# Performance work log

Measured on AMD Instinct MI355X. Metric: run time of the kernel, lower is better.

Reference implementation:

```python
import jax, jax.numpy as jnp
import numpy as np

N = 20000   # nodes per type (lnc and dis)
E = 160000  # edges per meta-path graph and per pos/neg link graph
H = 8       # attention heads
D = 32      # out_size per head (H*D = 256 flattened)
HID = 256   # hidden_size from ResNet projection


def _bn(x, g, b, eps=1e-5):
    # training-mode BatchNorm1d (biased variance, like torch)
    m = x.mean(0)
    v = x.var(0)
    return g * (x - m) * jax.lax.rsqrt(v + eps) + b


def _leaky(x, slope):
    return jnp.where(x >= 0, x, slope * x)


def _gat(h_src, h_dst, src, dst, W, al, ar, n_dst):
    # DGL GATConv (bipartite, shared fc, no bias, eval mode)
    fs = (h_src @ W).reshape(-1, H, D)          # [Ns,H,D]
    fd = (h_dst @ W).reshape(-1, H, D)          # [Nd,H,D]
    el = (fs * al).sum(-1)                      # [Ns,H]
    er = (fd * ar).sum(-1)                      # [Nd,H]
    e = _leaky(el[src] + er[dst], 0.2)          # [E,H]
    emax = jax.ops.segment_max(e, dst, num_segments=n_dst)
    emax = jnp.where(jnp.isfinite(emax), emax, 0.0)   # zero in-degree safety
    ee = jnp.exp(e - emax[dst])
    den = jax.ops.segment_sum(ee, dst, num_segments=n_dst)
    a = ee / jnp.maximum(den[dst], 1e-9)        # edge softmax over incoming edges
    out = jax.ops.segment_sum(a[:, :, None] * fs[src], dst, num_segments=n_dst)
    return _leaky(out, 0.01).reshape(n_dst, H * D)  # activation=F.leaky_relu, flatten(1)


def _sem_attn(z, W1, b1, w2):
    # z: [N, 2, H*D]; SemanticAttention
    w = (jnp.tanh(z @ W1 + b1) @ w2).mean(0)    # [2]
    beta = jax.nn.softmax(w, axis=0)            # [2]
    return (beta[None, :, None] * z).sum(1)     # [N, H*D]


def setup_inputs() -> dict:
    key = jax.random.key(0)
    ks = jax.random.split(key, 32)
    s = 0.05
    inp = {
        "x_lnc": jax.random.normal(ks[0], (N, 256), jnp.float32),
        "x_dis": jax.random.normal(ks[1], (N, 256), jnp.float32),
        "proj_W": jax.random.normal(ks[2], (2, 256, HID), jnp.float32) * s,
        "proj_bn_g": jnp.ones((HID,), jnp.float32),
        "proj_bn_b": jnp.zeros((HID,), jnp.float32),
        "short_W": jax.random.normal(ks[3], (2, 256, HID), jnp.float32) * s,
        "short_b": jnp.zeros((2, HID), jnp.float32),
        "gat_W": jax.random.normal(ks[4], (4, HID, H * D), jnp.float32) * s,
        "gat_al": jax.random.normal(ks[5], (4, H, D), jnp.float32) * s,
        "gat_ar": jax.random.normal(ks[6], (4, H, D), jnp.float32) * s,
        "sem_W1": jax.random.normal(ks[7], (H * D, 128), jnp.float32) * s,
        "sem_b1": jnp.zeros((128,), jnp.float32),
        "sem_w2": jax.random.normal(ks[8], (128,), jnp.float32) * s,
    }
    names = ["ld_src", "ld_dst", "ll_src", "ll_dst", "dl_src", "dl_dst",
             "dd_src", "dd_dst", "pos_src", "pos_dst", "neg_src", "neg_dst"]
    for i, nm in enumerate(names):
        inp[nm] = jax.random.randint(ks[10 + i], (E,), 0, N, jnp.int32)
    return inp


def reference(x_lnc, x_dis, proj_W, proj_bn_g, proj_bn_b, short_W, short_b,
              gat_W, gat_al, gat_ar, sem_W1, sem_b1, sem_w2,
              ld_src, ld_dst, ll_src, ll_dst, dl_src, dl_dst,
              dd_src, dd_dst, pos_src, pos_dst, neg_src, neg_dst):
    # ResNet projection (shared BN applied per-branch, training-mode stats)
    l_x = _leaky(_bn(x_lnc @ proj_W[0], proj_bn_g, proj_bn_b), 0.01) + (x_lnc @ short_W[0] + short_b[0])
    d_x = _leaky(_bn(x_dis @ proj_W[1], proj_bn_g, proj_bn_b), 0.01) + (x_dis @ short_W[1] + short_b[1])
    # HANLayer: 4 meta-path GATs with pairings (l,d),(l,l),(d,l),(d,d)
    e0 = _gat(l_x, d_x, ld_src, ld_dst, gat_W[0], gat_al[0], gat_ar[0], N)  # dst dis
    e1 = _gat(l_x, l_x, ll_src, ll_dst, gat_W[1], gat_al[1], gat_ar[1], N)  # dst lnc
    e2 = _gat(d_x, l_x, dl_src, dl_dst, gat_W[2], gat_al[2], gat_ar[2], N)  # dst lnc
    e3 = _gat(d_x, d_x, dd_src, dd_dst, gat_W[3], gat_al[3], gat_ar[3], N)  # dst dis
    l_embs = _sem_attn(jnp.stack((e1, e2), axis=1), sem_W1, sem_b1, sem_w2)
    d_embs = _sem_attn(jnp.stack((e0, e3), axis=1), sem_W1, sem_b1, sem_w2)
    # Hadamard u_mul_v over 'lnc-dis' edges (pos graph and neg graph)
    pos_z = l_embs[pos_src] * d_embs[pos_dst]
    neg_z = l_embs[neg_src] * d_embs[neg_dst]
    return pos_z, neg_z, l_embs, d_embs
```

## Files before the change

### kernel.cpp

```cpp
#include <hip/hip_runtime.h>
#include <math.h>

#define NN 20000
#define NE 160000
#define SLOT 40

typedef _Float16 f16;
typedef __attribute__((ext_vector_type(8))) _Float16 f16x8;
typedef __attribute__((ext_vector_type(4))) float f32x4;

__device__ __forceinline__ float leakyf(float x, float s){ return x >= 0.f ? x : s*x; }
__device__ __forceinline__ ushort f2h(float x){ f16 h = (f16)x; ushort u; __builtin_memcpy(&u,&h,2); return u; }
__device__ __forceinline__ float h2f(ushort u){ f16 h; __builtin_memcpy(&h,&u,2); return (float)h; }

__device__ __forceinline__ void gload_lds16(const void* g, void* l){
  __builtin_amdgcn_global_load_lds((const __attribute__((address_space(1))) uint*)g,
                                   (__attribute__((address_space(3))) uint*)l, 16, 0, 0);
}

__global__ __launch_bounds__(256) void prep(const float* __restrict__ x_lnc,
    const float* __restrict__ x_dis, const float* __restrict__ proj_W,
    const float* __restrict__ short_W, const float* __restrict__ gat_W,
    const float* __restrict__ sem_W1,
    ushort* __restrict__ xhl, ushort* __restrict__ xhd,
    ushort* btpl, ushort* btpd, ushort* btgl, ushort* btgd, ushort* btsm,
    int* __restrict__ zbuf){
  int b = blockIdx.x;
  if (b < 10000){
    const float* in = (b >= 5000) ? x_dis : x_lnc;
    ushort* out = (b >= 5000) ? xhd : xhl;
    long idx = (long)(b % 5000)*256 + threadIdx.x;
    long r = idx>>6; int c4 = (int)(idx&63)<<2;
    float4 v = *(const float4*)(in + r*256 + c4);
    ushort4 o; o.x=f2h(v.x); o.y=f2h(v.y); o.z=f2h(v.z); o.w=f2h(v.w);
    *(ushort4*)(out + r*256 + c4) = o;
  } else if (b < 12688){
    int idx = (b-10000)*256 + threadIdx.x;
    float v; ushort* out; int n, k;
    if (idx < 131072){
      n = idx>>8; k = idx&255; out = btpl;
      v = (n<256)? proj_W[(size_t)k*256+n] : short_W[(size_t)k*256+(n-256)];
    } else if (idx < 262144){
      int l = idx-131072; n = l>>8; k = l&255; out = btpd;
      v = (n<256)? proj_W[65536+(size_t)k*256+n] : short_W[65536+(size_t)k*256+(n-256)];
    } else if (idx < 458752){
      int l = idx-262144; n = l>>8; k = l&255; out = btgl;
      int sl = n>>8; const float* bb = gat_W + (sl==0?0:(sl==1?65536:131072));
      v = bb[(size_t)k*256 + (n&255)];
    } else if (idx < 655360){
      int l = idx-458752; n = l>>8; k = l&255; out = btgd;
      int sl = n>>8; const float* bb = gat_W + (sl==0?0:(sl==1?131072:196608));
      v = bb[(size_t)k*256 + (n&255)];
    } else {
      int l = idx-655360; n = l>>8; k = l&255; out = btsm;
      v = sem_W1[(size_t)k*128 + n];
    }
    out[(size_t)n*256 + k] = f2h(v);
  } else {
    int idx = (b-12688)*256 + threadIdx.x;
    if (idx < 81028) zbuf[idx] = 0;
  }
}

__global__ void scatter_slots(const int* s0, const int* s1, const int* s2, const int* s3,
    const int* d0, const int* d1, const int* d2, const int* d3,
    int* __restrict__ cnt, int* __restrict__ slots){
  int g = blockIdx.y;
  const int* src = (g==0)?s0:(g==1)?s1:(g==2)?s2:s3;
  const int* dst = (g==0)?d0:(g==1)?d1:(g==2)?d2:d3;
  int i = blockIdx.x*256 + threadIdx.x;
  if (i<NE){
    int d = dst[i];
    int p = atomicAdd(&cnt[g*NN + d], 1);
    slots[(size_t)(g*NN + d)*SLOT + p] = src[i];
  }
}

template<int EPI>
__global__ __launch_bounds__(256) void gemm16(
    const ushort* __restrict__ A0, const ushort* __restrict__ A1,
    const ushort* __restrict__ B0, const ushort* __restrict__ B1,
    ushort* __restrict__ C0, ushort* __restrict__ C1, int ldc, int M,
    float* __restrict__ sbuf,
    const float* __restrict__ gat_al, const float* __restrict__ gat_ar,
    float* __restrict__ elbase, float* __restrict__ erbase,
    const float* __restrict__ b1v, const float* __restrict__ w2v){
  const int z = blockIdx.z;
  const ushort* A = z ? A1 : A0;
  const ushort* Bt = z ? B1 : B0;
  ushort* C = z ? C1 : C0;
  __shared__ ushort sm[16384];
  char* smc = (char*)sm;
  const int tid = threadIdx.x;
  const int lane = tid & 63, wid = tid >> 6;
  const int wr = wid >> 1, wc = wid & 1;
  const int fr = lane & 15, fq = lane >> 4;
  const int brow = blockIdx.y*128, bcol = blockIdx.x*128;
  f32x4 acc[4][4];
  #pragma unroll
  for (int i=0;i<4;i++)
    #pragma unroll
    for (int j=0;j<4;j++) acc[i][j] = (f32x4){0.f,0.f,0.f,0.f};

  for (int k0 = 0; k0 < 256; k0 += 64){
    __syncthreads();
    #pragma unroll
    for (int cc = 0; cc < 8; cc++){
      int c = wid*8 + cc;
      int ch = c & 15;
      int rel = ch*1024 + lane*16;
      int row = rel >> 7;
      int scb = (rel & 127) ^ ((row & 7) << 4);
      const char* src;
      if (c < 16){
        int gr = brow + row; gr = (gr < M) ? gr : (M-1);
        src = (const char*)A + (size_t)gr*512 + k0*2 + scb;
      } else {
        src = (const char*)Bt + (size_t)(bcol + row)*512 + k0*2 + scb;
      }
      gload_lds16(src, smc + ((c<16)?0:16384) + ch*1024);
    }
    __syncthreads();
    #pragma unroll
    for (int ks = 0; ks < 2; ks++){
      f16x8 af[4], bfr[4];
      #pragma unroll
      for (int i=0;i<4;i++){
        int r = wr*64 + i*16 + fr;
        int koff = ks*32 + fq*8;
        int aoff = ((r<<7) + koff*2) ^ ((r&7)<<4);
        af[i] = *(const f16x8*)(smc + aoff);
        int n = wc*64 + i*16 + fr;
        int boff = ((n<<7) + koff*2) ^ ((n&7)<<4);
        bfr[i] = *(const f16x8*)(smc + 16384 + boff);
      }
      #pragma unroll
      for (int i=0;i<4;i++)
        #pragma unroll
        for (int j=0;j<4;j++)
          acc[i][j] = __builtin_amdgcn_mfma_f32_16x16x32_f16(af[i], bfr[j], acc[i][j], 0,0,0);
    }
  }

  if (EPI==1 || EPI==2){
    #pragma unroll
    for (int i=0;i<4;i++){
      #pragma unroll
      for (int e=0;e<4;e++){
        int gr = brow + wr*64 + i*16 + fq*4 + e;
        if (gr < M){
          #pragma unroll
          for (int j=0;j<4;j++)
            C[(size_t)gr*ldc + bcol + wc*64 + j*16 + fr] = f2h(acc[i][j][e]);
        }
      }
    }
  }

  if (EPI==1 && bcol < 256){
    float* gsum = sbuf + z*512;
    float* gsq  = gsum + 256;
    #pragma unroll
    for (int j=0;j<4;j++){
      float s=0.f, q=0.f;
      #pragma unroll
      for (int i=0;i<4;i++)
        #pragma unroll
        for (int e=0;e<4;e++){
          int gr = brow + wr*64 + i*16 + fq*4 + e;
          if (gr < M){ float v = acc[i][j][e]; s += v; q += v*v; }
        }
      s += __shfl_xor(s,16); s += __shfl_xor(s,32);
      q += __shfl_xor(q,16); q += __shfl_xor(q,32);
      if (fq==0){
        int gc = bcol + wc*64 + j*16 + fr;
        atomicAdd(&gsum[gc], s);
        atomicAdd(&gsq[gc], q);
      }
    }
  }

  if (EPI==2){
    int slice = bcol >> 8;
    int hbase = (bcol & 255) >> 5;
    float *d1=nullptr, *d2=nullptr; const float *a1=nullptr, *a2=nullptr;
    if (z==0){
      if (slice==0){ d1=elbase; a1=gat_al; }
      else if (slice==1){ d1=elbase+160000; a1=gat_al+256; d2=erbase+160000; a2=gat_ar+256; }
      else { d1=erbase+320000; a1=gat_ar+512; }
    } else {
      if (slice==0){ d1=erbase; a1=gat_ar; }
      else if (slice==1){ d1=elbase+320000; a1=gat_al+512; }
      else { d1=elbase+480000; a1=gat_al+768; d2=erbase+480000; a2=gat_ar+768; }
    }
    int hA = hbase + wc*2, hB = hA+1;
    #pragma unroll
    for (int t=0;t<2;t++){
      const float* av = t ? a2 : a1;
      float* dst = t ? d2 : d1;
      if (t==1 && d2==nullptr) break;
      float avv[4];
      #pragma unroll
      for (int j=0;j<4;j++)
        avv[j] = av[(hbase + wc*2 + (j>>1))*32 + (j&1)*16 + fr];
      #pragma unroll
      for (int i=0;i<4;i++){
        #pragma unroll
        for (int e=0;e<4;e++){
          int gr = brow + wr*64 + i*16 + fq*4 + e;
          float pA = acc[i][0][e]*avv[0] + acc[i][1][e]*avv[1];
          float pB = acc[i][2][e]*avv[2] + acc[i][3][e]*avv[3];
          pA += __shfl_xor(pA,1); pA += __shfl_xor(pA,2);
          pA += __shfl_xor(pA,4); pA += __shfl_xor(pA,8);
          pB += __shfl_xor(pB,1); pB += __shfl_xor(pB,2);
          pB += __shfl_xor(pB,4); pB += __shfl_xor(pB,8);
          if (fr==0 && gr < M){
            dst[(size_t)gr*8 + hA] = pA;
            dst[(size_t)gr*8 + hB] = pB;
          }
        }
      }
    }
  }

  if (EPI==3){
    float b1c[4], w2c[4];
    #pragma unroll
    for (int j=0;j<4;j++){
      int col = wc*64 + j*16 + fr;
      b1c[j] = b1v[col]; w2c[j] = w2v[col];
    }
    int segA = brow/20000;
    int bound = (segA+1)*20000;
    float t0=0.f, t1=0.f;
    #pragma unroll
    for (int i=0;i<4;i++){
      #pragma unroll
      for (int e=0;e<4;e++){
        int gr = brow + wr*64 + i*16 + fq*4 + e;
        float rs = 0.f;
        #pragma unroll
        for (int j=0;j<4;j++){
          float x = acc[i][j][e] + b1c[j];
          float ex = __expf(2.f*x);
          rs += (1.f - 2.f/(ex+1.f))*w2c[j];
        }
        if (gr < bound) t0 += rs; else t1 += rs;
      }
    }
    #pragma unroll
    for (int off=32; off>0; off>>=1){ t0 += __shfl_xor(t0,off); t1 += __shfl_xor(t1,off); }
    if (lane==0){
      atomicAdd(&sbuf[segA], t0);
      if (brow + 127 >= bound) atomicAdd(&sbuf[segA+1], t1);
    }
  }
}

__global__ __launch_bounds__(256) void proj_apply2(const ushort* __restrict__ PS_l,
    const ushort* __restrict__ PS_d, const float* __restrict__ sbuf,
    const float* __restrict__ gg, const float* __restrict__ bb,
    const float* __restrict__ short_b, ushort* __restrict__ out_l, ushort* __restrict__ out_d){
  int y = blockIdx.y;
  const ushort* PS = y ? PS_d : PS_l;
  ushort* out = y ? out_d : out_l;
  const float* gsum = sbuf + y*512;
  const float* gsq  = gsum + 256;
  const float* sb = short_b + y*256;
  long idx = (long)blockIdx.x*256 + threadIdx.x;
  long r = idx>>6; int c4 = (int)(idx&63)<<2;
  ushort4 pu = *(const ushort4*)(PS + r*512 + c4);
  ushort4 su = *(const ushort4*)(PS + r*512 + 256 + c4);
  float pv[4] = {h2f(pu.x),h2f(pu.y),h2f(pu.z),h2f(pu.w)};
  float sv[4] = {h2f(su.x),h2f(su.y),h2f(su.z),h2f(su.w)};
  ushort o[4];
  #pragma unroll
  for (int k=0;k<4;k++){
    int c = c4+k;
    float m = gsum[c]*(1.f/NN);
    float va = gsq[c]*(1.f/NN) - m*m;
    float ri = rsqrtf(va + 1e-5f);
    float yv = (pv[k]-m)*ri*gg[c] + bb[c];
    o[k] = f2h(leakyf(yv,0.01f) + sv[k] + sb[c]);
  }
  ushort4 ov; ov.x=o[0]; ov.y=o[1]; ov.z=o[2]; ov.w=o[3];
  *(ushort4*)(out + r*256 + c4) = ov;
}

__global__ __launch_bounds__(256) void gat_fused(const int* __restrict__ cnt,
    const int* __restrict__ slots, const float* __restrict__ elbase,
    const float* __restrict__ erbase, const ushort* __restrict__ fc_l,
    const ushort* __restrict__ fc_d, ushort* __restrict__ sems){
  const int g = blockIdx.y;
  const int n = blockIdx.x*4 + (threadIdx.x>>6);
  const int lane = threadIdx.x & 63;
  const int co[4]   = {0,256,256,512};
  const int semo[4] = {40000,0,20000,60000};
  const float* el = elbase + g*160000;
  const float* er = erbase + g*160000;
  const ushort* F = (g<2) ? fc_l : fc_d;
  const int coloff = co[g];
  const int j = lane>>3, h = lane&7, hc = lane>>3;
  const int e1 = cnt[g*NN + n];
  const long sb = (long)(g*NN + n)*SLOT;
  const float ern = er[n*8+h];
  float ssum = 0.f;
  float4 acc = make_float4(0.f,0.f,0.f,0.f);

  for (int base = 0; base < e1; base += 8){
    int idx = base + j;
    bool valid = idx < e1;
    int src = valid ? slots[sb + idx] : 0;
    float p = valid ? __expf(leakyf(el[src*8+h] + ern, 0.2f)) : 0.f;
    ssum += p;
    #pragma unroll
    for (int e=0;e<8;e++){
      if (base + e >= e1) break;
      float w = __shfl(p, e*8 + hc);
      int s = __shfl(src, e*8);
      ushort4 fu = *(const ushort4*)(F + (size_t)s*768 + coloff + lane*4);
      acc.x = fmaf(w,h2f(fu.x),acc.x); acc.y = fmaf(w,h2f(fu.y),acc.y);
      acc.z = fmaf(w,h2f(fu.z),acc.z); acc.w = fmaf(w,h2f(fu.w),acc.w);
    }
  }
  ssum += __shfl_xor(ssum,8); ssum += __shfl_xor(ssum,16); ssum += __shfl_xor(ssum,32);
  float rd = 1.f/fmaxf(__shfl(ssum, hc), 1e-9f);
  ushort4 o;
  o.x = f2h(leakyf(acc.x*rd, 0.01f)); o.y = f2h(leakyf(acc.y*rd, 0.01f));
  o.z = f2h(leakyf(acc.z*rd, 0.01f)); o.w = f2h(leakyf(acc.w*rd, 0.01f));
  *(ushort4*)(sems + (size_t)(semo[g]+n)*256 + lane*4) = o;
}

__global__ __launch_bounds__(256) void sem_combine(const ushort* __restrict__ sems,
    const float* __restrict__ tsum, float* __restrict__ lemb, float* __restrict__ demb,
    ushort* __restrict__ lemb16, ushort* __restrict__ demb16){
  float wl0 = tsum[0]*(1.f/20000.f), wl1 = tsum[1]*(1.f/20000.f);
  float m = fmaxf(wl0,wl1);
  float ea = __expf(wl0-m), eb = __expf(wl1-m);
  float b0 = ea/(ea+eb), b1 = eb/(ea+eb);
  float wd0 = tsum[2]*(1.f/20000.f), wd1 = tsum[3]*(1.f/20000.f);
  m = fmaxf(wd0,wd1);
  ea = __expf(wd0-m); eb = __expf(wd1-m);
  float b2 = ea/(ea+eb), b3 = eb/(ea+eb);

  long idx = (long)blockIdx.x*256 + threadIdx.x;
  long r = idx>>6; int c4 = (int)(idx&63)<<2;
  ushort4 v1 = *(const ushort4*)(sems + (r          )*256 + c4);
  ushort4 v2 = *(const ushort4*)(sems + (r + 20000L )*256 + c4);
  ushort4 v0 = *(const ushort4*)(sems + (r + 40000L )*256 + c4);
  ushort4 v3 = *(const ushort4*)(sems + (r + 60000L )*256 + c4);
  float4 lo, dd;
  lo.x = b0*h2f(v1.x) + b1*h2f(v2.x); dd.x = b2*h2f(v0.x) + b3*h2f(v3.x);
  lo.y = b0*h2f(v1.y) + b1*h2f(v2.y); dd.y = b2*h2f(v0.y) + b3*h2f(v3.y);
  lo.z = b0*h2f(v1.z) + b1*h2f(v2.z); dd.z = b2*h2f(v0.z) + b3*h2f(v3.z);
  lo.w = b0*h2f(v1.w) + b1*h2f(v2.w); dd.w = b2*h2f(v0.w) + b3*h2f(v3.w);
  *(float4*)(lemb + r*256 + c4) = lo;
  *(float4*)(demb + r*256 + c4) = dd;
  ushort4 lh, dh;
  lh.x=f2h(lo.x); lh.y=f2h(lo.y); lh.z=f2h(lo.z); lh.w=f2h(lo.w);
  dh.x=f2h(dd.x); dh.y=f2h(dd.y); dh.z=f2h(dd.z); dh.w=f2h(dd.w);
  *(ushort4*)(lemb16 + r*256 + c4) = lh;
  *(ushort4*)(demb16 + r*256 + c4) = dh;
}

__global__ __launch_bounds__(256) void edge_mul2(const int* __restrict__ ps, const int* __restrict__ pd,
    const int* __restrict__ ns, const int* __restrict__ nd,
    const ushort* __restrict__ lemb16, const ushort* __restrict__ demb16,
    float* __restrict__ pos, float* __restrict__ neg){
  long idx = (long)blockIdx.x*256 + threadIdx.x;
  const long H = (long)NE*64;
  const int *es, *ed; float* out; long t;
  if (idx < H){ es=ps; ed=pd; out=pos; t=idx; }
  else { es=ns; ed=nd; out=neg; t=idx-H; }
  long i = t>>6; int jj = (int)(t&63);
  int s = es[i], d = ed[i];
  ushort4 a = *(const ushort4*)(lemb16 + (size_t)s*256 + (size_t)jj*4);
  ushort4 b = *(const ushort4*)(demb16 + (size_t)d*256 + (size_t)jj*4);
  float4 o = make_float4(h2f(a.x)*h2f(b.x), h2f(a.y)*h2f(b.y),
                         h2f(a.z)*h2f(b.z), h2f(a.w)*h2f(b.w));
  *(float4*)(out + (size_t)t*4) = o;
}

extern "C" void kernel_launch(void* const* d_in, const int* in_sizes, int n_in,
                              void* d_out, int out_size, void* d_ws, size_t ws_size,
                              hipStream_t stream){
  const float* x_lnc  = (const float*)d_in[0];
  const float* x_dis  = (const float*)d_in[1];
  const float* proj_W = (const float*)d_in[2];
  const float* bn_g   = (const float*)d_in[3];
  const float* bn_b   = (const float*)d_in[4];
  const float* short_W= (const float*)d_in[5];
  const float* short_b= (const float*)d_in[6];
  const float* gat_W  = (const float*)d_in[7];
  const float* gat_al = (const float*)d_in[8];
  const float* gat_ar = (const float*)d_in[9];
  const float* sem_W1 = (const float*)d_in[10];
  const float* sem_b1 = (const float*)d_in[11];
  const float* sem_w2 = (const float*)d_in[12];
  const int* g_src[4] = {(const int*)d_in[13],(const int*)d_in[15],(const int*)d_in[17],(const int*)d_in[19]};
  const int* g_dst[4] = {(const int*)d_in[14],(const int*)d_in[16],(const int*)d_in[18],(const int*)d_in[20]};
  const int* pos_src = (const int*)d_in[21];
  const int* pos_dst = (const int*)d_in[22];
  const int* neg_src = (const int*)d_in[23];
  const int* neg_dst = (const int*)d_in[24];

  const long LEMB = (long)NN*256;
  const long EOUT = (long)NE*256;

  float* outf = (float*)d_out;
  float* pos  = outf;
  float* negr = outf + EOUT;
  float* lemb = outf + 2*EOUT;
  float* demb = lemb + LEMB;

  ushort* PS_l = (ushort*)negr;
  ushort* PS_d = PS_l + 10240000;
  ushort* fc_l = (ushort*)negr;
  ushort* fc_d = fc_l + 15360000;

  float* ws   = (float*)d_ws;
  float* sbuf = ws;
  float* tsum = ws + 1024;
  int*   cnt  = (int*)(ws + 1028);
  float* elbase = ws + 81028;
  float* erbase = elbase + 640000;
  int*   slots  = (int*)(erbase + 640000);
  ushort* xhl  = (ushort*)(slots + 3200000);
  ushort* xhd  = xhl + 5120000;
  ushort* axl  = xhd + 5120000;
  ushort* axd  = axl + 5120000;
  ushort* sems = axd + 5120000;
  ushort* lemb16 = sems + 20480000;
  ushort* demb16 = lemb16 + 5120000;
  ushort* btpl = demb16 + 5120000;
  ushort* btpd = btpl + 131072;
  ushort* btgl = btpd + 131072;
  ushort* btgd = btgl + 196608;
  ushort* btsm = btgd + 196608;

  prep<<<13005,256,0,stream>>>(x_lnc, x_dis, proj_W, short_W, gat_W, sem_W1,
                               xhl, xhd, btpl, btpd, btgl, btgd, btsm, (int*)ws);
  scatter_slots<<<dim3(625,4),256,0,stream>>>(g_src[0],g_src[1],g_src[2],g_src[3],
      g_dst[0],g_dst[1],g_dst[2],g_dst[3], cnt, slots);

  gemm16<1><<<dim3(4,157,2),256,0,stream>>>(xhl, xhd, btpl, btpd, PS_l, PS_d, 512, NN,
      sbuf, nullptr, nullptr, nullptr, nullptr, nullptr, nullptr);
  proj_apply2<<<dim3(5000,2),256,0,stream>>>(PS_l, PS_d, sbuf, bn_g, bn_b, short_b, axl, axd);

  gemm16<2><<<dim3(6,157,2),256,0,stream>>>(axl, axd, btgl, btgd, fc_l, fc_d, 768, NN,
      nullptr, gat_al, gat_ar, elbase, erbase, nullptr, nullptr);

  gat_fused<<<dim3(5000,4),256,0,stream>>>(cnt, slots, elbase, erbase, fc_l, fc_d, sems);

  gemm16<3><<<dim3(1,625,1),256,0,stream>>>(sems, nullptr, btsm, nullptr, nullptr, nullptr, 128, 80000,
      tsum, nullptr, nullptr, nullptr, nullptr, sem_b1, sem_w2);

  sem_combine<<<5000,256,0,stream>>>(sems, tsum, lemb, demb, lemb16, demb16);

  edge_mul2<<<80000,256,0,stream>>>(pos_src, pos_dst, neg_src, neg_dst, lemb16, demb16, pos, negr);
}
```

Baseline: 405.6 us.

## Fold GAT attention vectors into the weight matrix as extra GEMM columns

Precomputes W·a_l and W·a_r per head in the prep kernel and appends them as 32 extra output columns of the GAT projection GEMM. The el/er attention logits then come straight out of the MFMA accumulators, replacing the shuffle-reduction epilogue. The gat_fused kernel reads the new packed [N,32] logit layout. It also drops the early break in the inner aggregation loop, so invalid edges run with zero weight. The cost is an extra column tile per GEMM, mostly padding, plus fp16-rounded folded weights that slightly change the logits' precision.

```diff
diff --git a/kernel.cpp b/kernel.cpp
--- a/kernel.cpp
+++ b/kernel.cpp
@@ -21,6 +21,7 @@
 __global__ __launch_bounds__(256) void prep(const float* __restrict__ x_lnc,
     const float* __restrict__ x_dis, const float* __restrict__ proj_W,
     const float* __restrict__ short_W, const float* __restrict__ gat_W,
+    const float* __restrict__ gat_al, const float* __restrict__ gat_ar,
     const float* __restrict__ sem_W1,
     ushort* __restrict__ xhl, ushort* __restrict__ xhd,
     ushort* btpl, ushort* btpd, ushort* btgl, ushort* btgd, ushort* btsm,
@@ -56,8 +57,35 @@
       v = sem_W1[(size_t)k*128 + n];
     }
     out[(size_t)n*256 + k] = f2h(v);
+  } else if (b < 12752){
+    int idx = (b-12688)*256 + threadIdx.x;
+    int side = idx >> 13;
+    int r = idx & 8191;
+    int c = r >> 8;
+    int k = r & 255;
+    int h = c & 7, sel = c >> 3;
+    int gi; const float* av;
+    if (side==0){
+      gi = (sel==0)?0:((sel==3)?2:1);
+      av = (sel<=1)? gat_al : gat_ar;
+    } else {
+      gi = (sel==0)?0:((sel==1)?2:3);
+      av = (sel==1||sel==2)? gat_al : gat_ar;
+    }
+    const float* wrow = gat_W + gi*65536 + (size_t)k*256 + h*32;
+    const float* a = av + gi*256 + h*32;
+    float s = 0.f;
+    #pragma unroll
+    for (int d=0; d<32; d++) s += wrow[d]*a[d];
+    ushort* out = side ? btgd : btgl;
+    out[(size_t)(768+c)*256 + k] = f2h(s);
+  } else if (b < 12848){
+    int idx = (b-12752)*256 + threadIdx.x;
+    uint* pl = (uint*)(btgl + 800*256);
+    uint* pd = (uint*)(btgd + 800*256);
+    if (idx < 12288) pl[idx] = 0; else pd[idx-12288] = 0;
   } else {
-    int idx = (b-12688)*256 + threadIdx.x;
+    int idx = (b-12848)*256 + threadIdx.x;
     if (idx < 81028) zbuf[idx] = 0;
   }
 }
@@ -82,8 +110,7 @@
     const ushort* __restrict__ B0, const ushort* __restrict__ B1,
     ushort* __restrict__ C0, ushort* __restrict__ C1, int ldc, int M,
     float* __restrict__ sbuf,
-    const float* __restrict__ gat_al, const float* __restrict__ gat_ar,
-    float* __restrict__ elbase, float* __restrict__ erbase,
+    float* __restrict__ elr_l, float* __restrict__ elr_d,
     const float* __restrict__ b1v, const float* __restrict__ w2v){
   const int z = blockIdx.z;
   const ushort* A = z ? A1 : A0;
@@ -142,7 +169,7 @@
     }
   }
 
-  if (EPI==1 || EPI==2){
+  if (EPI==1 || (EPI==2 && bcol < 768)){
     #pragma unroll
     for (int i=0;i<4;i++){
       #pragma unroll
@@ -152,6 +179,21 @@
           #pragma unroll
           for (int j=0;j<4;j++)
             C[(size_t)gr*ldc + bcol + wc*64 + j*16 + fr] = f2h(acc[i][j][e]);
+        }
+      }
+    }
+  }
+
+  if (EPI==2 && bcol >= 768 && wc == 0){
+    float* elr = z ? elr_d : elr_l;
+    #pragma unroll
+    for (int i=0;i<4;i++){
+      #pragma unroll
+      for (int e=0;e<4;e++){
+        int gr = brow + wr*64 + i*16 + fq*4 + e;
+        if (gr < M){
+          elr[(size_t)gr*32 + fr]      = acc[i][0][e];
+          elr[(size_t)gr*32 + 16 + fr] = acc[i][1][e];
         }
       }
     }
@@ -176,49 +218,6 @@
         int gc = bcol + wc*64 + j*16 + fr;
         atomicAdd(&gsum[gc], s);
         atomicAdd(&gsq[gc], q);
-      }
-    }
-  }
-
-  if (EPI==2){
-    int slice = bcol >> 8;
-    int hbase = (bcol & 255) >> 5;
-    float *d1=nullptr, *d2=nullptr; const float *a1=nullptr, *a2=nullptr;
-    if (z==0){
-      if (slice==0){ d1=elbase; a1=gat_al; }
-      else if (slice==1){ d1=elbase+160000; a1=gat_al+256; d2=erbase+160000; a2=gat_ar+256; }
-      else { d1=erbase+320000; a1=gat_ar+512; }
-    } else {
-      if (slice==0){ d1=erbase; a1=gat_ar; }
-      else if (slice==1){ d1=elbase+320000; a1=gat_al+512; }
-      else { d1=elbase+480000; a1=gat_al+768; d2=erbase+480000; a2=gat_ar+768; }
-    }
-    int hA = hbase + wc*2, hB = hA+1;
-    #pragma unroll
-    for (int t=0;t<2;t++){
-      const float* av = t ? a2 : a1;
-      float* dst = t ? d2 : d1;
-      if (t==1 && d2==nullptr) break;
-      float avv[4];
-      #pragma unroll
-      for (int j=0;j<4;j++)
-        avv[j] = av[(hbase + wc*2 + (j>>1))*32 + (j&1)*16 + fr];
-      #pragma unroll
-      for (int i=0;i<4;i++){
-        #pragma unroll
-        for (int e=0;e<4;e++){
-          int gr = brow + wr*64 + i*16 + fq*4 + e;
-          float pA = acc[i][0][e]*avv[0] + acc[i][1][e]*avv[1];
-          float pB = acc[i][2][e]*avv[2] + acc[i][3][e]*avv[3];
-          pA += __shfl_xor(pA,1); pA += __shfl_xor(pA,2);
-          pA += __shfl_xor(pA,4); pA += __shfl_xor(pA,8);
-          pB += __shfl_xor(pB,1); pB += __shfl_xor(pB,2);
-          pB += __shfl_xor(pB,4); pB += __shfl_xor(pB,8);
-          if (fr==0 && gr < M){
-            dst[(size_t)gr*8 + hA] = pA;
-            dst[(size_t)gr*8 + hB] = pB;
-          }
-        }
       }
     }
   }
@@ -288,22 +287,25 @@
 }
 
 __global__ __launch_bounds__(256) void gat_fused(const int* __restrict__ cnt,
-    const int* __restrict__ slots, const float* __restrict__ elbase,
-    const float* __restrict__ erbase, const ushort* __restrict__ fc_l,
+    const int* __restrict__ slots, const float* __restrict__ elr_l,
+    const float* __restrict__ elr_d, const ushort* __restrict__ fc_l,
     const ushort* __restrict__ fc_d, ushort* __restrict__ sems){
   const int g = blockIdx.y;
   const int n = blockIdx.x*4 + (threadIdx.x>>6);
   const int lane = threadIdx.x & 63;
-  const int co[4]   = {0,256,256,512};
-  const int semo[4] = {40000,0,20000,60000};
-  const float* el = elbase + g*160000;
-  const float* er = erbase + g*160000;
+  const int co[4]    = {0,256,256,512};
+  const int semo[4]  = {40000,0,20000,60000};
+  const int eloA[4]  = {0,8,8,16};
+  const int eroA[4]  = {0,16,24,24};
+  const float* elb = (g<2) ? elr_l : elr_d;
+  const float* erb = (g==1||g==2) ? elr_l : elr_d;
+  const int eloff = eloA[g], eroff = eroA[g];
   const ushort* F = (g<2) ? fc_l : fc_d;
   const int coloff = co[g];
   const int j = lane>>3, h = lane&7, hc = lane>>3;
   const int e1 = cnt[g*NN + n];
   const long sb = (long)(g*NN + n)*SLOT;
-  const float ern = er[n*8+h];
+  const float ern = erb[(size_t)n*32 + eroff + h];
   float ssum = 0.f;
   float4 acc = make_float4(0.f,0.f,0.f,0.f);
 
@@ -311,11 +313,10 @@
     int idx = base + j;
     bool valid = idx < e1;
     int src = valid ? slots[sb + idx] : 0;
-    float p = valid ? __expf(leakyf(el[src*8+h] + ern, 0.2f)) : 0.f;
+    float p = valid ? __expf(leakyf(elb[(size_t)src*32 + eloff + h] + ern, 0.2f)) : 0.f;
     ssum += p;
     #pragma unroll
     for (int e=0;e<8;e++){
-      if (base + e >= e1) break;
       float w = __shfl(p, e*8 + hc);
       int s = __shfl(src, e*8);
       ushort4 fu = *(const ushort4*)(F + (size_t)s*768 + coloff + lane*4);
@@ -422,9 +423,9 @@
   float* sbuf = ws;
   float* tsum = ws + 1024;
   int*   cnt  = (int*)(ws + 1028);
-  float* elbase = ws + 81028;
-  float* erbase = elbase + 640000;
-  int*   slots  = (int*)(erbase + 640000);
+  float* elr_l = ws + 81028;
+  float* elr_d = elr_l + 640000;
+  int*   slots  = (int*)(elr_d + 640000);
   ushort* xhl  = (ushort*)(slots + 3200000);
   ushort* xhd  = xhl + 5120000;
   ushort* axl  = xhd + 5120000;
@@ -435,25 +436,25 @@
   ushort* btpl = demb16 + 5120000;
   ushort* btpd = btpl + 131072;
   ushort* btgl = btpd + 131072;
-  ushort* btgd = btgl + 196608;
-  ushort* btsm = btgd + 196608;
-
-  prep<<<13005,256,0,stream>>>(x_lnc, x_dis, proj_W, short_W, gat_W, sem_W1,
-                               xhl, xhd, btpl, btpd, btgl, btgd, btsm, (int*)ws);
+  ushort* btgd = btgl + 229376;
+  ushort* btsm = btgd + 229376;
+
+  prep<<<13165,256,0,stream>>>(x_lnc, x_dis, proj_W, short_W, gat_W, gat_al, gat_ar,
+                               sem_W1, xhl, xhd, btpl, btpd, btgl, btgd, btsm, (int*)ws);
   scatter_slots<<<dim3(625,4),256,0,stream>>>(g_src[0],g_src[1],g_src[2],g_src[3],
       g_dst[0],g_dst[1],g_dst[2],g_dst[3], cnt, slots);
 
   gemm16<1><<<dim3(4,157,2),256,0,stream>>>(xhl, xhd, btpl, btpd, PS_l, PS_d, 512, NN,
-      sbuf, nullptr, nullptr, nullptr, nullptr, nullptr, nullptr);
+      sbuf, nullptr, nullptr, nullptr, nullptr);
   proj_apply2<<<dim3(5000,2),256,0,stream>>>(PS_l, PS_d, sbuf, bn_g, bn_b, short_b, axl, axd);
 
-  gemm16<2><<<dim3(6,157,2),256,0,stream>>>(axl, axd, btgl, btgd, fc_l, fc_d, 768, NN,
-      nullptr, gat_al, gat_ar, elbase, erbase, nullptr, nullptr);
-
-  gat_fused<<<dim3(5000,4),256,0,stream>>>(cnt, slots, elbase, erbase, fc_l, fc_d, sems);
+  gemm16<2><<<dim3(7,157,2),256,0,stream>>>(axl, axd, btgl, btgd, fc_l, fc_d, 768, NN,
+      nullptr, elr_l, elr_d, nullptr, nullptr);
+
+  gat_fused<<<dim3(5000,4),256,0,stream>>>(cnt, slots, elr_l, elr_d, fc_l, fc_d, sems);
 
   gemm16<3><<<dim3(1,625,1),256,0,stream>>>(sems, nullptr, btsm, nullptr, nullptr, nullptr, 128, 80000,
-      tsum, nullptr, nullptr, nullptr, nullptr, sem_b1, sem_w2);
+      tsum, nullptr, nullptr, sem_b1, sem_w2);
 
   sem_combine<<<5000,256,0,stream>>>(sems, tsum, lemb, demb, lemb16, demb16);
 
```

After: 386.7 us. -4.7%, faster.
